# Kernel optimization log

Measured on AMD Instinct MI355X. Metric: run time of the kernel, lower is better.

Reference implementation:

```python
import jax, jax.numpy as jnp
import numpy as np

N, E, B = 50000, 800000, 64
ND, ED, HID, NC = 64, 16, 128, 6
HEADS = [4, 4, 1]
CH = [32, 32, 128]
CONCAT = [True, True, False]

PNAMES = ['pW', 'pb'] + [f'{p}{l}' for l in range(3) for p in ['W', 'as', 'ad', 'ae', 'We', 'b', 'g', 'be']] + ['gW1', 'gb1', 'gW2', 'gb2', 'cW1', 'cb1', 'cW2', 'cb2']


def _gat_conv(x, src, dst, ea, W, a_s, a_d, a_e, We, b, heads, ch, concat):
    n = x.shape[0]
    xp = (x @ W).reshape(n, heads, ch)          # [N,H,C]
    al_src = (xp * a_s).sum(-1)                 # [N,H]
    al_dst = (xp * a_d).sum(-1)                 # [N,H]
    ep = (ea @ We).reshape(-1, heads, ch)       # [E,H,C]
    al_edge = (ep * a_e).sum(-1)                # [E,H]
    alpha = jax.nn.leaky_relu(al_src[src] + al_dst[dst] + al_edge, 0.2)
    # segment softmax over destination nodes
    amax = jax.ops.segment_max(alpha, dst, num_segments=n)
    ex = jnp.exp(alpha - amax[dst])
    den = jax.ops.segment_sum(ex, dst, num_segments=n)
    alpha = ex / (den[dst] + 1e-16)
    out = jax.ops.segment_sum(xp[src] * alpha[:, :, None], dst, num_segments=n)
    out = out.reshape(n, heads * ch) if concat else out.mean(axis=1)
    return out + b


def _layernorm(x, g, be):
    m = x.mean(-1, keepdims=True)
    v = ((x - m) ** 2).mean(-1, keepdims=True)
    return (x - m) / jnp.sqrt(v + 1e-5) * g + be


def _forward(x, edge_index, edge_attr, batch, params):
    src, dst = edge_index[0], edge_index[1]
    h = jax.nn.relu(x @ params['pW'] + params['pb'])
    for l in range(3):
        r = h
        h = _gat_conv(h, src, dst, edge_attr, params[f'W{l}'], params[f'as{l}'],
                      params[f'ad{l}'], params[f'ae{l}'], params[f'We{l}'], params[f'b{l}'],
                      HEADS[l], CH[l], CONCAT[l])
        h = _layernorm(h, params[f'g{l}'], params[f'be{l}'])
        h = jax.nn.elu(h)
        h = h + r
    # GlobalAttention pooling: gate MLP + segment softmax over graphs
    gate = jax.nn.relu(h @ params['gW1'] + params['gb1']) @ params['gW2'] + params['gb2']  # [N,1]
    gmax = jax.ops.segment_max(gate, batch, num_segments=B)
    ge = jnp.exp(gate - gmax[batch])
    gden = jax.ops.segment_sum(ge, batch, num_segments=B)
    att = ge / (gden[batch] + 1e-16)
    pooled = jax.ops.segment_sum(att * h, batch, num_segments=B)  # [B,HID]
    return jax.nn.relu(pooled @ params['cW1'] + params['cb1']) @ params['cW2'] + params['cb2']


def setup_inputs() -> dict:
    key = jax.random.key(0)
    ks = iter(jax.random.split(key, 64))
    nx = lambda: next(ks)
    rn = lambda shape, s=0.1: jax.random.normal(nx(), shape, jnp.float32) * s
    inp = {
        'x': jax.random.normal(nx(), (N, ND), jnp.float32),
        'edge_index': jax.random.randint(nx(), (2, E), 0, N),
        'edge_attr': jax.random.normal(nx(), (E, ED), jnp.float32),
        'batch': jnp.sort(jax.random.randint(nx(), (N,), 0, B)),
        'pW': rn((ND, HID)), 'pb': jnp.zeros((HID,), jnp.float32),
    }
    for l in range(3):
        h, c = HEADS[l], CH[l]
        inp[f'W{l}'] = rn((HID, h * c))
        inp[f'as{l}'] = rn((h, c))
        inp[f'ad{l}'] = rn((h, c))
        inp[f'ae{l}'] = rn((h, c))
        inp[f'We{l}'] = rn((ED, h * c))
        inp[f'b{l}'] = jnp.zeros((HID,), jnp.float32)
        inp[f'g{l}'] = jnp.ones((HID,), jnp.float32)
        inp[f'be{l}'] = jnp.zeros((HID,), jnp.float32)
    inp['gW1'] = rn((HID, HID // 2)); inp['gb1'] = jnp.zeros((HID // 2,), jnp.float32)
    inp['gW2'] = rn((HID // 2, 1)); inp['gb2'] = jnp.zeros((1,), jnp.float32)
    inp['cW1'] = rn((HID, HID // 2)); inp['cb1'] = jnp.zeros((HID // 2,), jnp.float32)
    inp['cW2'] = rn((HID // 2, NC)); inp['cb2'] = jnp.zeros((NC,), jnp.float32)
    return inp


def reference(x, edge_index, edge_attr, batch, pW, pb,
              W0, as0, ad0, ae0, We0, b0, g0, be0,
              W1, as1, ad1, ae1, We1, b1, g1, be1,
              W2, as2, ad2, ae2, We2, b2, g2, be2,
              gW1, gb1, gW2, gb2, cW1, cb1, cW2, cb2):
    params = dict(zip(PNAMES, (pW, pb, W0, as0, ad0, ae0, We0, b0, g0, be0,
                               W1, as1, ad1, ae1, We1, b1, g1, be1,
                               W2, as2, ad2, ae2, We2, b2, g2, be2,
                               gW1, gb1, gW2, gb2, cW1, cb1, cW2, cb2)))
    return _forward(x, edge_index, edge_attr, batch, params)
```

## Files before the change

kernel.cpp:

```cpp
#include <hip/hip_runtime.h>
#include <hip/hip_fp16.h>
#include <math.h>

#define N_NODES 50000
#define N_EDGES 800000
#define NB      64
#define ND      64
#define ED      16
#define HID     128
#define NC      6
#define POOL_SPLIT 32
#define SCAN_BLOCKS ((N_NODES + 255) / 256)
#define GEMM_BLOCKS ((N_NODES + 63) / 64)

typedef _Float16 f16;
typedef f16  half8  __attribute__((ext_vector_type(8)));
typedef float floatx4 __attribute__((ext_vector_type(4)));

__global__ void k_setup(const float* __restrict__ pW, const float* __restrict__ W0,
                        const float* __restrict__ W1, const float* __restrict__ W2,
                        const float* __restrict__ We0, const float* __restrict__ ae0,
                        const float* __restrict__ We1, const float* __restrict__ ae1,
                        const float* __restrict__ We2, const float* __restrict__ ae2,
                        int* __restrict__ deg, float* __restrict__ pooled,
                        float* __restrict__ WeAe,
                        f16* __restrict__ Wtp, f16* __restrict__ Wt0,
                        f16* __restrict__ Wt1, f16* __restrict__ Wt2) {
    int i = blockIdx.x * 256 + threadIdx.x;
    if (i < N_NODES) deg[i] = 0;
    if (i < NB * HID) pooled[i] = 0.f;
    if (i < 128 * 64) {
        int n = i / 64, k = i % 64;
        Wtp[i] = (f16)pW[k * 128 + n];
    }
    if (i < 128 * 128) {
        int n = i / 128, k = i % 128;
        Wt0[i] = (f16)W0[k * 128 + n];
        Wt1[i] = (f16)W1[k * 128 + n];
        Wt2[i] = (f16)W2[k * 128 + n];
    }
    if (i >= 60000 && i < 60144) {
        int t = i - 60000;
        if (t < 64) {
            int k = t >> 2, h = t & 3;
            float s = 0.f;
            for (int c = 0; c < 32; c++) s += We0[k * HID + h * 32 + c] * ae0[h * 32 + c];
            WeAe[k * 9 + h] = s;
        } else if (t < 128) {
            int tt = t - 64;
            int k = tt >> 2, h = tt & 3;
            float s = 0.f;
            for (int c = 0; c < 32; c++) s += We1[k * HID + h * 32 + c] * ae1[h * 32 + c];
            WeAe[k * 9 + 4 + h] = s;
        } else {
            int k = t - 128;
            float s = 0.f;
            for (int c = 0; c < HID; c++) s += We2[k * HID + c] * ae2[c];
            WeAe[k * 9 + 8] = s;
        }
    }
}

template <int K, int MODE>
__global__ __launch_bounds__(256) void k_gemm(
        const float* __restrict__ act, const f16* __restrict__ Wt,
        const float* __restrict__ bias, const float* __restrict__ as_,
        const float* __restrict__ ad_, float* __restrict__ hout,
        __half* __restrict__ xp, float* __restrict__ al_src,
        float* __restrict__ al_dst) {
    constexpr int KP = K + 8;
    __shared__ __align__(16) f16 A[64 * KP];
    __shared__ float part_s[4][64];
    __shared__ float part_d[4][64];
    int tid = threadIdx.x;
    int base = blockIdx.x * 64;

    constexpr int NV = 64 * K / 4 / 256;
    #pragma unroll
    for (int i = 0; i < NV; i++) {
        int v = tid + i * 256;
        int row = v / (K / 4);
        int k4 = v % (K / 4);
        float4 xv = make_float4(0.f, 0.f, 0.f, 0.f);
        if (base + row < N_NODES)
            xv = *(const float4*)(act + (size_t)(base + row) * K + k4 * 4);
        f16* dp = &A[row * KP + k4 * 4];
        dp[0] = (f16)xv.x; dp[1] = (f16)xv.y; dp[2] = (f16)xv.z; dp[3] = (f16)xv.w;
    }
    __syncthreads();

    int w = tid >> 6, l = tid & 63;
    int lm = l & 15, q = l >> 4;
    floatx4 acc[4][2];
    #pragma unroll
    for (int mt = 0; mt < 4; mt++)
        #pragma unroll
        for (int j = 0; j < 2; j++)
            acc[mt][j] = (floatx4){0.f, 0.f, 0.f, 0.f};

    #pragma unroll
    for (int kt = 0; kt < K / 32; kt++) {
        int ko = kt * 32 + q * 8;
        half8 b0 = *(const half8*)(Wt + (size_t)(w * 32 + lm) * K + ko);
        half8 b1 = *(const half8*)(Wt + (size_t)(w * 32 + 16 + lm) * K + ko);
        #pragma unroll
        for (int mt = 0; mt < 4; mt++) {
            half8 a = *(const half8*)(&A[(mt * 16 + lm) * KP + ko]);
            acc[mt][0] = __builtin_amdgcn_mfma_f32_16x16x32_f16(a, b0, acc[mt][0], 0, 0, 0);
            acc[mt][1] = __builtin_amdgcn_mfma_f32_16x16x32_f16(a, b1, acc[mt][1], 0, 0, 0);
        }
    }

    if (MODE == 0) {
        float b0 = bias[w * 32 + lm];
        float b1 = bias[w * 32 + 16 + lm];
        #pragma unroll
        for (int mt = 0; mt < 4; mt++)
            #pragma unroll
            for (int r = 0; r < 4; r++) {
                int row = mt * 16 + q * 4 + r;
                if (base + row < N_NODES) {
                    hout[(size_t)(base + row) * HID + w * 32 + lm]      = fmaxf(acc[mt][0][r] + b0, 0.f);
                    hout[(size_t)(base + row) * HID + w * 32 + 16 + lm] = fmaxf(acc[mt][1][r] + b1, 0.f);
                }
            }
    } else {
        float a0 = as_[w * 32 + lm], a1 = as_[w * 32 + 16 + lm];
        float e0 = ad_[w * 32 + lm], e1 = ad_[w * 32 + 16 + lm];
        float ps[4][4], pd[4][4];
        #pragma unroll
        for (int mt = 0; mt < 4; mt++)
            #pragma unroll
            for (int r = 0; r < 4; r++) {
                ps[mt][r] = acc[mt][0][r] * a0 + acc[mt][1][r] * a1;
                pd[mt][r] = acc[mt][0][r] * e0 + acc[mt][1][r] * e1;
            }
        #pragma unroll
        for (int off = 1; off < 16; off <<= 1)
            #pragma unroll
            for (int mt = 0; mt < 4; mt++)
                #pragma unroll
                for (int r = 0; r < 4; r++) {
                    ps[mt][r] += __shfl_xor(ps[mt][r], off, 64);
                    pd[mt][r] += __shfl_xor(pd[mt][r], off, 64);
                }
        if (MODE == 1) {
            if (lm == 0)
                #pragma unroll
                for (int mt = 0; mt < 4; mt++)
                    #pragma unroll
                    for (int r = 0; r < 4; r++) {
                        int n = base + mt * 16 + q * 4 + r;
                        if (n < N_NODES) {
                            al_src[n * 4 + w] = ps[mt][r];
                            al_dst[n * 4 + w] = pd[mt][r];
                        }
                    }
        } else {
            if (lm == 0)
                #pragma unroll
                for (int mt = 0; mt < 4; mt++)
                    #pragma unroll
                    for (int r = 0; r < 4; r++) {
                        part_s[w][mt * 16 + q * 4 + r] = ps[mt][r];
                        part_d[w][mt * 16 + q * 4 + r] = pd[mt][r];
                    }
        }
        __syncthreads();
        #pragma unroll
        for (int mt = 0; mt < 4; mt++)
            #pragma unroll
            for (int r = 0; r < 4; r++) {
                int row = mt * 16 + q * 4 + r;
                A[row * KP + w * 32 + lm]      = (f16)acc[mt][0][r];
                A[row * KP + w * 32 + 16 + lm] = (f16)acc[mt][1][r];
            }
        if (MODE == 2 && tid < 64) {
            int n = base + tid;
            if (n < N_NODES) {
                al_src[n] = part_s[0][tid] + part_s[1][tid] + part_s[2][tid] + part_s[3][tid];
                al_dst[n] = part_d[0][tid] + part_d[1][tid] + part_d[2][tid] + part_d[3][tid];
            }
        }
        __syncthreads();
        #pragma unroll
        for (int i = 0; i < 4; i++) {
            int v = tid + i * 256;
            int row = v >> 4, c8 = v & 15;
            if (base + row < N_NODES) {
                float4 hv = *(const float4*)(&A[row * KP + c8 * 8]);
                *reinterpret_cast<float4*>(reinterpret_cast<char*>(xp) +
                    ((size_t)(base + row) * HID + c8 * 8) * 2) = hv;
            }
        }
    }
}

__global__ void k_deg(const int* __restrict__ dst, int* __restrict__ deg,
                      int* __restrict__ rank) {
    int e = blockIdx.x * blockDim.x + threadIdx.x;
    if (e < N_EDGES) rank[e] = atomicAdd(&deg[dst[e]], 1);
}

__global__ void k_scanA(const int* __restrict__ deg, int* __restrict__ bsum) {
    __shared__ int wsu[4];
    int t = threadIdx.x;
    int i = blockIdx.x * 256 + t;
    int d = (i < N_NODES) ? deg[i] : 0;
    int v = d;
    #pragma unroll
    for (int o = 32; o > 0; o >>= 1) v += __shfl_xor(v, o, 64);
    if ((t & 63) == 0) wsu[t >> 6] = v;
    __syncthreads();
    if (t == 0) bsum[blockIdx.x] = wsu[0] + wsu[1] + wsu[2] + wsu[3];
}

__global__ void k_scanB(const int* __restrict__ bsum, int* __restrict__ bpre,
                        int* __restrict__ offs) {
    __shared__ int sc[256];
    int t = threadIdx.x;
    int d = (t < SCAN_BLOCKS) ? bsum[t] : 0;
    sc[t] = d;
    __syncthreads();
    for (int o = 1; o < 256; o <<= 1) {
        int v = (t >= o) ? sc[t - o] : 0;
        __syncthreads();
        sc[t] += v;
        __syncthreads();
    }
    if (t < SCAN_BLOCKS) bpre[t] = sc[t] - d;
    if (t == 0) offs[N_NODES] = N_EDGES;
}

__global__ void k_scanC(const int* __restrict__ deg, const int* __restrict__ bpre,
                        int* __restrict__ offs) {
    __shared__ int sc[256];
    int t = threadIdx.x;
    int i = blockIdx.x * 256 + t;
    int d = (i < N_NODES) ? deg[i] : 0;
    sc[t] = d;
    __syncthreads();
    for (int o = 1; o < 256; o <<= 1) {
        int v = (t >= o) ? sc[t - o] : 0;
        __syncthreads();
        sc[t] += v;
        __syncthreads();
    }
    if (i < N_NODES) offs[i] = bpre[blockIdx.x] + sc[t] - d;
}

__global__ void k_edge_build(const int* __restrict__ src, const int* __restrict__ dst,
                             const int* __restrict__ rank, const int* __restrict__ offs,
                             const float* __restrict__ ea, const float* __restrict__ WeAe,
                             float4* __restrict__ rec) {
    __shared__ float w[ED * 9];
    __shared__ float4 rs[256][4];
    __shared__ int rp[256];
    int tid = threadIdx.x;
    if (tid < ED * 9) w[tid] = WeAe[tid];
    __syncthreads();
    int e = blockIdx.x * 256 + tid;
    if (e < N_EDGES) {
        float ev[ED];
        const float4* ep4 = reinterpret_cast<const float4*>(ea + (size_t)e * ED);
        #pragma unroll
        for (int q = 0; q < 4; q++) {
            float4 v = ep4[q];
            ev[q * 4 + 0] = v.x; ev[q * 4 + 1] = v.y;
            ev[q * 4 + 2] = v.z; ev[q * 4 + 3] = v.w;
        }
        float r[9];
        #pragma unroll
        for (int j = 0; j < 9; j++) r[j] = 0.f;
        #pragma unroll
        for (int k = 0; k < ED; k++) {
            float evk = ev[k];
            #pragma unroll
            for (int j = 0; j < 9; j++) r[j] += evk * w[k * 9 + j];
        }
        int d = dst[e], s = src[e];
        rp[tid] = offs[d] + rank[e];
        rs[tid][0] = make_float4(r[0], r[1], r[2], r[3]);
        rs[tid][1] = make_float4(r[4], r[5], r[6], r[7]);
        rs[tid][2] = make_float4(r[8], __int_as_float(s), __int_as_float(d), 0.f);
        rs[tid][3] = make_float4(0.f, 0.f, 0.f, 0.f);
    } else {
        rp[tid] = -1;
    }
    __syncthreads();
    int g0 = tid >> 2, q = tid & 3;
    #pragma unroll
    for (int rr = 0; rr < 4; rr++) {
        int g = rr * 64 + g0;
        int p = rp[g];
        if (p >= 0) rec[(size_t)p * 4 + q] = rs[g][q];
    }
}

template <int H, int SLOT>
__global__ void k_node_agg(const int* __restrict__ offs, const float4* __restrict__ rec,
                           const float* __restrict__ al_src, const float* __restrict__ al_dst,
                           const __half* __restrict__ xp, const float* __restrict__ bias,
                           const float* __restrict__ g, const float* __restrict__ be,
                           const float* __restrict__ hin, float* __restrict__ hout) {
    int tid = threadIdx.x;
    int wave = tid >> 6;
    int lane = tid & 63;
    int n = blockIdx.x * 4 + wave;
    if (n >= N_NODES) return;
    int e0 = offs[n], e1 = offs[n + 1];
    int side = lane >> 4;
    int cl = lane & 15;
    int c = cl * 8;
    int h = cl >> 2;
    float ald = (H == 4) ? al_dst[n * 4 + h] : al_dst[n];
    float acc[8] = {0.f, 0.f, 0.f, 0.f, 0.f, 0.f, 0.f, 0.f};
    float den = 0.f;

    auto fetchw = [&](int i, int& s, float& wv) {
        if (i < e1) {
            const float* rb = (const float*)(rec + (size_t)i * 4);
            s = __float_as_int(rb[9]);
            float r = (H == 4) ? rb[SLOT * 4 + h] : rb[8];
            float al = ((H == 4) ? al_src[s * 4 + h] : al_src[s]) + ald + r;
            al = (al >= 0.f) ? al : 0.2f * al;
            wv = __expf(al);
        } else { s = 0; wv = 0.f; }
    };
    auto accum = [&](uint4 r, float wv) {
        union { uint4 u; __half2 h2[4]; } t2; t2.u = r;
        #pragma unroll
        for (int j = 0; j < 4; j++) {
            float2 f = __half22float2(t2.h2[j]);
            acc[j * 2]     += wv * f.x;
            acc[j * 2 + 1] += wv * f.y;
        }
        den += wv;
    };

    int i = e0 + side;
    int sA, sB; float wA, wB;
    fetchw(i, sA, wA);
    fetchw(i + 4, sB, wB);
    while (i < e1) {
        uint4 rA = *reinterpret_cast<const uint4*>(xp + (size_t)sA * HID + c);
        uint4 rB = *reinterpret_cast<const uint4*>(xp + (size_t)sB * HID + c);
        int sC, sD; float wC, wD;
        fetchw(i + 8, sC, wC);
        fetchw(i + 12, sD, wD);
        accum(rA, wA);
        accum(rB, wB);
        sA = sC; wA = wC; sB = sD; wB = wD;
        i += 8;
    }
    #pragma unroll
    for (int j = 0; j < 8; j++) {
        acc[j] += __shfl_xor(acc[j], 16, 64);
        acc[j] += __shfl_xor(acc[j], 32, 64);
    }
    den += __shfl_xor(den, 16, 64);
    den += __shfl_xor(den, 32, 64);

    float inv = 1.f / (den + 1e-16f);
    float v[8];
    const float4 bv0 = *reinterpret_cast<const float4*>(bias + c);
    const float4 bv1 = *reinterpret_cast<const float4*>(bias + c + 4);
    v[0] = acc[0] * inv + bv0.x; v[1] = acc[1] * inv + bv0.y;
    v[2] = acc[2] * inv + bv0.z; v[3] = acc[3] * inv + bv0.w;
    v[4] = acc[4] * inv + bv1.x; v[5] = acc[5] * inv + bv1.y;
    v[6] = acc[6] * inv + bv1.z; v[7] = acc[7] * inv + bv1.w;
    float s8 = v[0] + v[1] + v[2] + v[3] + v[4] + v[5] + v[6] + v[7];
    #pragma unroll
    for (int o = 8; o > 0; o >>= 1) s8 += __shfl_xor(s8, o, 64);
    float mean = s8 * (1.f / HID);
    float q8 = 0.f;
    float d[8];
    #pragma unroll
    for (int j = 0; j < 8; j++) { d[j] = v[j] - mean; q8 += d[j] * d[j]; }
    #pragma unroll
    for (int o = 8; o > 0; o >>= 1) q8 += __shfl_xor(q8, o, 64);
    float rstd = rsqrtf(q8 * (1.f / HID) + 1e-5f);
    if (side < 2) {
        int co = c + side * 4;
        int j0 = side * 4;
        const float4 gv  = *reinterpret_cast<const float4*>(g + co);
        const float4 bev = *reinterpret_cast<const float4*>(be + co);
        float y0 = d[j0]     * rstd * gv.x + bev.x;
        float y1 = d[j0 + 1] * rstd * gv.y + bev.y;
        float y2 = d[j0 + 2] * rstd * gv.z + bev.z;
        float y3 = d[j0 + 3] * rstd * gv.w + bev.w;
        y0 = (y0 > 0.f) ? y0 : (__expf(y0) - 1.f);
        y1 = (y1 > 0.f) ? y1 : (__expf(y1) - 1.f);
        y2 = (y2 > 0.f) ? y2 : (__expf(y2) - 1.f);
        y3 = (y3 > 0.f) ? y3 : (__expf(y3) - 1.f);
        const float4 rv = *reinterpret_cast<const float4*>(hin + (size_t)n * HID + co);
        *reinterpret_cast<float4*>(hout + (size_t)n * HID + co) =
            make_float4(y0 + rv.x, y1 + rv.y, y2 + rv.z, y3 + rv.w);
    }
}

__global__ void k_gate(const float* __restrict__ h, const float* __restrict__ gW1,
                       const float* __restrict__ gb1, const float* __restrict__ gW2,
                       const float* __restrict__ gb2, const int* __restrict__ batch,
                       float* __restrict__ gate, int* __restrict__ goff) {
    __shared__ float hs[16][HID];
    int tid = threadIdx.x;
    int base = blockIdx.x * 16;
    if (tid < 16) {
        int n = base + tid;
        int cur = batch[n];
        int prev = (n == 0) ? -1 : batch[n - 1];
        for (int gg = prev + 1; gg <= cur; gg++) goff[gg] = n;
        if (n == N_NODES - 1)
            for (int gg = cur + 1; gg <= NB; gg++) goff[gg] = N_NODES;
    }
    for (int idx = tid; idx < 16 * HID; idx += 256) {
        int nn = idx >> 7, k = idx & 127;
        hs[nn][k] = h[(size_t)(base + nn) * HID + k];
    }
    __syncthreads();
    int c = tid & 63;
    int wave = tid >> 6;
    float acc[4] = {0.f, 0.f, 0.f, 0.f};
    #pragma unroll 8
    for (int k = 0; k < HID; k++) {
        float wv = gW1[k * 64 + c];
        #pragma unroll
        for (int q = 0; q < 4; q++) acc[q] += hs[wave * 4 + q][k] * wv;
    }
    float b1 = gb1[c], w2 = gW2[c];
    float p[4];
    #pragma unroll
    for (int q = 0; q < 4; q++) p[q] = fmaxf(acc[q] + b1, 0.f) * w2;
    #pragma unroll
    for (int o = 32; o > 0; o >>= 1) {
        #pragma unroll
        for (int q = 0; q < 4; q++) p[q] += __shfl_xor(p[q], o, 64);
    }
    if (c == 0) {
        float b2 = gb2[0];
        #pragma unroll
        for (int q = 0; q < 4; q++) gate[base + wave * 4 + q] = p[q] + b2;
    }
}

__global__ void k_gmaxden(const float* __restrict__ gate, const int* __restrict__ goff,
                          float* __restrict__ gmax, float* __restrict__ gden) {
    int b = blockIdx.x;
    int t = threadIdx.x;
    __shared__ float red[256];
    int s = goff[b], e = goff[b + 1];
    float m = -__builtin_inff();
    for (int n = s + t; n < e; n += 256) m = fmaxf(m, gate[n]);
    red[t] = m;
    __syncthreads();
    for (int o = 128; o > 0; o >>= 1) { if (t < o) red[t] = fmaxf(red[t], red[t + o]); __syncthreads(); }
    m = red[0];
    __syncthreads();
    float d = 0.f;
    for (int n = s + t; n < e; n += 256) d += __expf(gate[n] - m);
    red[t] = d;
    __syncthreads();
    for (int o = 128; o > 0; o >>= 1) { if (t < o) red[t] += red[t + o]; __syncthreads(); }
    if (t == 0) { gmax[b] = m; gden[b] = red[0]; }
}

__global__ void k_pool(const float* __restrict__ h, const float* __restrict__ gate,
                       const float* __restrict__ gmax, const float* __restrict__ gden,
                       const int* __restrict__ goff, float* __restrict__ pooled) {
    int b = blockIdx.x;
    int part = blockIdx.y;
    int c = threadIdx.x;
    int s = goff[b], e = goff[b + 1];
    float m = gmax[b];
    float dinv = 1.f / (gden[b] + 1e-16f);
    float acc = 0.f;
    for (int n = s + part; n < e; n += POOL_SPLIT) {
        float att = __expf(gate[n] - m) * dinv;
        acc += att * h[(size_t)n * HID + c];
    }
    atomicAdd(&pooled[b * HID + c], acc);
}

__global__ void k_head(const float* __restrict__ pooled, const float* __restrict__ cW1,
                       const float* __restrict__ cb1, const float* __restrict__ cW2,
                       const float* __restrict__ cb2, float* __restrict__ out) {
    int b = blockIdx.x;
    int t = threadIdx.x;
    __shared__ float pr[HID];
    __shared__ float tr[64];
    pr[t] = pooled[b * HID + t];
    pr[t + 64] = pooled[b * HID + t + 64];
    __syncthreads();
    float a = cb1[t];
    #pragma unroll 8
    for (int k = 0; k < HID; k++) a += pr[k] * cW1[k * 64 + t];
    tr[t] = fmaxf(a, 0.f);
    __syncthreads();
    if (t < NC) {
        float o = cb2[t];
        #pragma unroll
        for (int k = 0; k < 64; k++) o += tr[k] * cW2[k * NC + t];
        out[b * NC + t] = o;
    }
}

extern "C" void kernel_launch(void* const* d_in, const int* in_sizes, int n_in,
                              void* d_out, int out_size, void* d_ws, size_t ws_size,
                              hipStream_t stream) {
    (void)in_sizes; (void)n_in; (void)out_size; (void)ws_size;
    const float* x     = (const float*)d_in[0];
    const int*   ei    = (const int*)d_in[1];
    const float* ea    = (const float*)d_in[2];
    const int*   batch = (const int*)d_in[3];
    const float* pW    = (const float*)d_in[4];
    const float* pb    = (const float*)d_in[5];
    const float *W[3], *as_[3], *ad_[3], *ae_[3], *We[3], *bb[3], *gg[3], *be[3];
    for (int l = 0; l < 3; l++) {
        int base = 6 + 8 * l;
        W[l]   = (const float*)d_in[base + 0];
        as_[l] = (const float*)d_in[base + 1];
        ad_[l] = (const float*)d_in[base + 2];
        ae_[l] = (const float*)d_in[base + 3];
        We[l]  = (const float*)d_in[base + 4];
        bb[l]  = (const float*)d_in[base + 5];
        gg[l]  = (const float*)d_in[base + 6];
        be[l]  = (const float*)d_in[base + 7];
    }
    const float* gW1 = (const float*)d_in[30];
    const float* gb1 = (const float*)d_in[31];
    const float* gW2 = (const float*)d_in[32];
    const float* gb2 = (const float*)d_in[33];
    const float* cW1 = (const float*)d_in[34];
    const float* cb1 = (const float*)d_in[35];
    const float* cW2 = (const float*)d_in[36];
    const float* cb2 = (const float*)d_in[37];
    float* out = (float*)d_out;

    char* p = (char*)d_ws;
    auto take = [&](size_t bytes) -> char* {
        char* r = p;
        p += (bytes + 255) & ~(size_t)255;
        return r;
    };
    float*  h0      = (float*)take((size_t)N_NODES * HID * 4);
    float*  h1      = (float*)take((size_t)N_NODES * HID * 4);
    __half* xp      = (__half*)take((size_t)N_NODES * HID * 2);
    float*  al_src  = (float*)take((size_t)N_NODES * 4 * 4);
    float*  al_dst  = (float*)take((size_t)N_NODES * 4 * 4);
    float4* rec     = (float4*)take((size_t)N_EDGES * 64);
    int*    deg     = (int*)take((size_t)N_NODES * 4);
    int*    offs    = (int*)take((size_t)(N_NODES + 1) * 4);
    int*    rank    = (int*)take((size_t)N_EDGES * 4);
    int*    bsum    = (int*)take(256 * 4);
    int*    bpre    = (int*)take(256 * 4);
    float*  WeAe    = (float*)take(ED * 9 * 4);
    float*  gate    = (float*)take((size_t)N_NODES * 4);
    float*  gmax    = (float*)take(NB * 4);
    float*  gden    = (float*)take(NB * 4);
    int*    goff    = (int*)take((NB + 1) * 4);
    float*  pooled  = (float*)take(NB * HID * 4);
    f16*    Wtp     = (f16*)take(128 * 64 * 2);
    f16*    Wt0     = (f16*)take(128 * 128 * 2);
    f16*    Wt1     = (f16*)take(128 * 128 * 2);
    f16*    Wt2     = (f16*)take(128 * 128 * 2);
    f16*    Wt[3]   = {Wt0, Wt1, Wt2};

    const int* src = ei;
    const int* dst = ei + N_EDGES;

    k_setup<<<256, 256, 0, stream>>>(pW, W[0], W[1], W[2], We[0], ae_[0], We[1], ae_[1],
                                     We[2], ae_[2], deg, pooled, WeAe, Wtp, Wt0, Wt1, Wt2);
    k_gemm<64, 0><<<GEMM_BLOCKS, 256, 0, stream>>>(x, Wtp, pb, nullptr, nullptr,
                                                   h0, nullptr, nullptr, nullptr);
    k_deg<<<(N_EDGES + 255) / 256, 256, 0, stream>>>(dst, deg, rank);
    k_scanA<<<SCAN_BLOCKS, 256, 0, stream>>>(deg, bsum);
    k_scanB<<<1, 256, 0, stream>>>(bsum, bpre, offs);
    k_scanC<<<SCAN_BLOCKS, 256, 0, stream>>>(deg, bpre, offs);
    k_edge_build<<<(N_EDGES + 255) / 256, 256, 0, stream>>>(src, dst, rank, offs, ea, WeAe, rec);

    float* hc = h0;
    float* hn = h1;
    k_gemm<128, 1><<<GEMM_BLOCKS, 256, 0, stream>>>(hc, Wt[0], nullptr, as_[0], ad_[0],
                                                    nullptr, xp, al_src, al_dst);
    k_node_agg<4, 0><<<(N_NODES + 3) / 4, 256, 0, stream>>>(offs, rec, al_src, al_dst, xp,
                                                            bb[0], gg[0], be[0], hc, hn);
    { float* t = hc; hc = hn; hn = t; }
    k_gemm<128, 1><<<GEMM_BLOCKS, 256, 0, stream>>>(hc, Wt[1], nullptr, as_[1], ad_[1],
                                                    nullptr, xp, al_src, al_dst);
    k_node_agg<4, 1><<<(N_NODES + 3) / 4, 256, 0, stream>>>(offs, rec, al_src, al_dst, xp,
                                                            bb[1], gg[1], be[1], hc, hn);
    { float* t = hc; hc = hn; hn = t; }
    k_gemm<128, 2><<<GEMM_BLOCKS, 256, 0, stream>>>(hc, Wt[2], nullptr, as_[2], ad_[2],
                                                    nullptr, xp, al_src, al_dst);
    k_node_agg<1, 0><<<(N_NODES + 3) / 4, 256, 0, stream>>>(offs, rec, al_src, al_dst, xp,
                                                            bb[2], gg[2], be[2], hc, hn);
    { float* t = hc; hc = hn; hn = t; }

    k_gate<<<N_NODES / 16, 256, 0, stream>>>(hc, gW1, gb1, gW2, gb2, batch, gate, goff);
    k_gmaxden<<<NB, 256, 0, stream>>>(gate, goff, gmax, gden);
    k_pool<<<dim3(NB, POOL_SPLIT), HID, 0, stream>>>(hc, gate, gmax, gden, goff, pooled);
    k_head<<<NB, 64, 0, stream>>>(pooled, cW1, cb1, cW2, cb2, out);
}
```

Before: 494.9 us.

## Store hidden activations in fp16, fuse projection with degree count, merge scans, deepen gather prefetch

```diff
diff --git a/kernel.cpp b/kernel.cpp
--- a/kernel.cpp
+++ b/kernel.cpp
@@ -12,6 +12,7 @@
 #define POOL_SPLIT 32
 #define SCAN_BLOCKS ((N_NODES + 255) / 256)
 #define GEMM_BLOCKS ((N_NODES + 63) / 64)
+#define DEG_BLOCKS  ((N_EDGES + 255) / 256)
 
 typedef _Float16 f16;
 typedef f16  half8  __attribute__((ext_vector_type(8)));
@@ -61,31 +62,44 @@
     }
 }
 
-template <int K, int MODE>
-__global__ __launch_bounds__(256) void k_gemm(
-        const float* __restrict__ act, const f16* __restrict__ Wt,
+template <int K, int MODE, typename AT>
+__device__ __forceinline__ void gemm_body(
+        const AT* __restrict__ act, const f16* __restrict__ Wt,
         const float* __restrict__ bias, const float* __restrict__ as_,
-        const float* __restrict__ ad_, float* __restrict__ hout,
+        const float* __restrict__ ad_, __half* __restrict__ hout,
         __half* __restrict__ xp, float* __restrict__ al_src,
-        float* __restrict__ al_dst) {
+        float* __restrict__ al_dst, int blk) {
     constexpr int KP = K + 8;
-    __shared__ __align__(16) f16 A[64 * KP];
+    constexpr int OP = HID + 8;
+    __shared__ __align__(16) f16 A[64 * OP];
     __shared__ float part_s[4][64];
     __shared__ float part_d[4][64];
     int tid = threadIdx.x;
-    int base = blockIdx.x * 64;
-
-    constexpr int NV = 64 * K / 4 / 256;
-    #pragma unroll
-    for (int i = 0; i < NV; i++) {
-        int v = tid + i * 256;
-        int row = v / (K / 4);
-        int k4 = v % (K / 4);
-        float4 xv = make_float4(0.f, 0.f, 0.f, 0.f);
-        if (base + row < N_NODES)
-            xv = *(const float4*)(act + (size_t)(base + row) * K + k4 * 4);
-        f16* dp = &A[row * KP + k4 * 4];
-        dp[0] = (f16)xv.x; dp[1] = (f16)xv.y; dp[2] = (f16)xv.z; dp[3] = (f16)xv.w;
+    int base = blk * 64;
+
+    if constexpr (sizeof(AT) == 4) {
+        constexpr int NV = 64 * (K / 4) / 256;
+        #pragma unroll
+        for (int i = 0; i < NV; i++) {
+            int v = tid + i * 256;
+            int row = v / (K / 4), k4 = v % (K / 4);
+            float4 xv = make_float4(0.f, 0.f, 0.f, 0.f);
+            if (base + row < N_NODES)
+                xv = *(const float4*)((const float*)act + (size_t)(base + row) * K + k4 * 4);
+            f16* dp = &A[row * KP + k4 * 4];
+            dp[0] = (f16)xv.x; dp[1] = (f16)xv.y; dp[2] = (f16)xv.z; dp[3] = (f16)xv.w;
+        }
+    } else {
+        constexpr int NV = 64 * (K / 8) / 256;
+        #pragma unroll
+        for (int i = 0; i < NV; i++) {
+            int v = tid + i * 256;
+            int row = v / (K / 8), k8 = v % (K / 8);
+            uint4 xv = make_uint4(0, 0, 0, 0);
+            if (base + row < N_NODES)
+                xv = *(const uint4*)((const __half*)act + (size_t)(base + row) * K + k8 * 8);
+            *(uint4*)(&A[row * KP + k8 * 8]) = xv;
+        }
     }
     __syncthreads();
 
@@ -114,16 +128,26 @@
     if (MODE == 0) {
         float b0 = bias[w * 32 + lm];
         float b1 = bias[w * 32 + 16 + lm];
+        __syncthreads();
         #pragma unroll
         for (int mt = 0; mt < 4; mt++)
             #pragma unroll
             for (int r = 0; r < 4; r++) {
                 int row = mt * 16 + q * 4 + r;
-                if (base + row < N_NODES) {
-                    hout[(size_t)(base + row) * HID + w * 32 + lm]      = fmaxf(acc[mt][0][r] + b0, 0.f);
-                    hout[(size_t)(base + row) * HID + w * 32 + 16 + lm] = fmaxf(acc[mt][1][r] + b1, 0.f);
-                }
+                A[row * OP + w * 32 + lm]      = (f16)fmaxf(acc[mt][0][r] + b0, 0.f);
+                A[row * OP + w * 32 + 16 + lm] = (f16)fmaxf(acc[mt][1][r] + b1, 0.f);
             }
+        __syncthreads();
+        #pragma unroll
+        for (int i = 0; i < 4; i++) {
+            int v = tid + i * 256;
+            int row = v >> 4, c8 = v & 15;
+            if (base + row < N_NODES) {
+                float4 hv = *(const float4*)(&A[row * OP + c8 * 8]);
+                *reinterpret_cast<float4*>(reinterpret_cast<char*>(hout) +
+                    ((size_t)(base + row) * HID + c8 * 8) * 2) = hv;
+            }
+        }
     } else {
         float a0 = as_[w * 32 + lm], a1 = as_[w * 32 + 16 + lm];
         float e0 = ad_[w * 32 + lm], e1 = ad_[w * 32 + 16 + lm];
@@ -172,8 +196,8 @@
             #pragma unroll
             for (int r = 0; r < 4; r++) {
                 int row = mt * 16 + q * 4 + r;
-                A[row * KP + w * 32 + lm]      = (f16)acc[mt][0][r];
-                A[row * KP + w * 32 + 16 + lm] = (f16)acc[mt][1][r];
+                A[row * OP + w * 32 + lm]      = (f16)acc[mt][0][r];
+                A[row * OP + w * 32 + 16 + lm] = (f16)acc[mt][1][r];
             }
         if (MODE == 2 && tid < 64) {
             int n = base + tid;
@@ -188,7 +212,7 @@
             int v = tid + i * 256;
             int row = v >> 4, c8 = v & 15;
             if (base + row < N_NODES) {
-                float4 hv = *(const float4*)(&A[row * KP + c8 * 8]);
+                float4 hv = *(const float4*)(&A[row * OP + c8 * 8]);
                 *reinterpret_cast<float4*>(reinterpret_cast<char*>(xp) +
                     ((size_t)(base + row) * HID + c8 * 8) * 2) = hv;
             }
@@ -196,10 +220,26 @@
     }
 }
 
-__global__ void k_deg(const int* __restrict__ dst, int* __restrict__ deg,
-                      int* __restrict__ rank) {
-    int e = blockIdx.x * blockDim.x + threadIdx.x;
-    if (e < N_EDGES) rank[e] = atomicAdd(&deg[dst[e]], 1);
+__global__ __launch_bounds__(256) void k_proj_deg(
+        const float* __restrict__ x, const f16* __restrict__ Wtp,
+        const float* __restrict__ pb, __half* __restrict__ h,
+        const int* __restrict__ dst, int* __restrict__ deg, int* __restrict__ rank) {
+    if (blockIdx.x < GEMM_BLOCKS) {
+        gemm_body<64, 0, float>(x, Wtp, pb, nullptr, nullptr, h, nullptr, nullptr, nullptr,
+                                blockIdx.x);
+    } else {
+        int e = (blockIdx.x - GEMM_BLOCKS) * 256 + threadIdx.x;
+        if (e < N_EDGES) rank[e] = atomicAdd(&deg[dst[e]], 1);
+    }
+}
+
+template <int K, int MODE>
+__global__ __launch_bounds__(256) void k_gemm(
+        const __half* __restrict__ act, const f16* __restrict__ Wt,
+        const float* __restrict__ as_, const float* __restrict__ ad_,
+        __half* __restrict__ xp, float* __restrict__ al_src, float* __restrict__ al_dst) {
+    gemm_body<K, MODE, __half>(act, Wt, nullptr, as_, ad_, nullptr, xp, al_src, al_dst,
+                               blockIdx.x);
 }
 
 __global__ void k_scanA(const int* __restrict__ deg, int* __restrict__ bsum) {
@@ -215,11 +255,19 @@
     if (t == 0) bsum[blockIdx.x] = wsu[0] + wsu[1] + wsu[2] + wsu[3];
 }
 
-__global__ void k_scanB(const int* __restrict__ bsum, int* __restrict__ bpre,
-                        int* __restrict__ offs) {
+__global__ void k_scanC2(const int* __restrict__ deg, const int* __restrict__ bsum,
+                         int* __restrict__ offs) {
     __shared__ int sc[256];
+    __shared__ int wred[4];
     int t = threadIdx.x;
-    int d = (t < SCAN_BLOCKS) ? bsum[t] : 0;
+    int b = (t < (int)blockIdx.x) ? bsum[t] : 0;
+    #pragma unroll
+    for (int o = 32; o > 0; o >>= 1) b += __shfl_xor(b, o, 64);
+    if ((t & 63) == 0) wred[t >> 6] = b;
+    __syncthreads();
+    int pre = wred[0] + wred[1] + wred[2] + wred[3];
+    int i = blockIdx.x * 256 + t;
+    int d = (i < N_NODES) ? deg[i] : 0;
     sc[t] = d;
     __syncthreads();
     for (int o = 1; o < 256; o <<= 1) {
@@ -228,25 +276,8 @@
         sc[t] += v;
         __syncthreads();
     }
-    if (t < SCAN_BLOCKS) bpre[t] = sc[t] - d;
-    if (t == 0) offs[N_NODES] = N_EDGES;
-}
-
-__global__ void k_scanC(const int* __restrict__ deg, const int* __restrict__ bpre,
-                        int* __restrict__ offs) {
-    __shared__ int sc[256];
-    int t = threadIdx.x;
-    int i = blockIdx.x * 256 + t;
-    int d = (i < N_NODES) ? deg[i] : 0;
-    sc[t] = d;
-    __syncthreads();
-    for (int o = 1; o < 256; o <<= 1) {
-        int v = (t >= o) ? sc[t - o] : 0;
-        __syncthreads();
-        sc[t] += v;
-        __syncthreads();
-    }
-    if (i < N_NODES) offs[i] = bpre[blockIdx.x] + sc[t] - d;
+    if (i < N_NODES) offs[i] = pre + sc[t] - d;
+    if (i == 0) offs[N_NODES] = N_EDGES;
 }
 
 __global__ void k_edge_build(const int* __restrict__ src, const int* __restrict__ dst,
@@ -302,7 +333,7 @@
                            const float* __restrict__ al_src, const float* __restrict__ al_dst,
                            const __half* __restrict__ xp, const float* __restrict__ bias,
                            const float* __restrict__ g, const float* __restrict__ be,
-                           const float* __restrict__ hin, float* __restrict__ hout) {
+                           const __half* __restrict__ hin, __half* __restrict__ hout) {
     int tid = threadIdx.x;
     int wave = tid >> 6;
     int lane = tid & 63;
@@ -339,19 +370,28 @@
     };
 
     int i = e0 + side;
-    int sA, sB; float wA, wB;
+    int sA, sB, sC, sD; float wA, wB, wC, wD;
     fetchw(i, sA, wA);
     fetchw(i + 4, sB, wB);
+    fetchw(i + 8, sC, wC);
+    fetchw(i + 12, sD, wD);
     while (i < e1) {
         uint4 rA = *reinterpret_cast<const uint4*>(xp + (size_t)sA * HID + c);
         uint4 rB = *reinterpret_cast<const uint4*>(xp + (size_t)sB * HID + c);
-        int sC, sD; float wC, wD;
-        fetchw(i + 8, sC, wC);
-        fetchw(i + 12, sD, wD);
+        uint4 rC = *reinterpret_cast<const uint4*>(xp + (size_t)sC * HID + c);
+        uint4 rD = *reinterpret_cast<const uint4*>(xp + (size_t)sD * HID + c);
+        int tA, tB, tC, tD; float vA, vB, vC, vD;
+        fetchw(i + 16, tA, vA);
+        fetchw(i + 20, tB, vB);
+        fetchw(i + 24, tC, vC);
+        fetchw(i + 28, tD, vD);
         accum(rA, wA);
         accum(rB, wB);
-        sA = sC; wA = wC; sB = sD; wB = wD;
-        i += 8;
+        accum(rC, wC);
+        accum(rD, wD);
+        sA = tA; wA = vA; sB = tB; wB = vB;
+        sC = tC; wC = vC; sD = tD; wD = vD;
+        i += 16;
     }
     #pragma unroll
     for (int j = 0; j < 8; j++) {
@@ -393,13 +433,18 @@
         y1 = (y1 > 0.f) ? y1 : (__expf(y1) - 1.f);
         y2 = (y2 > 0.f) ? y2 : (__expf(y2) - 1.f);
         y3 = (y3 > 0.f) ? y3 : (__expf(y3) - 1.f);
-        const float4 rv = *reinterpret_cast<const float4*>(hin + (size_t)n * HID + co);
-        *reinterpret_cast<float4*>(hout + (size_t)n * HID + co) =
-            make_float4(y0 + rv.x, y1 + rv.y, y2 + rv.z, y3 + rv.w);
-    }
-}
-
-__global__ void k_gate(const float* __restrict__ h, const float* __restrict__ gW1,
+        uint2 ru = *reinterpret_cast<const uint2*>(hin + (size_t)n * HID + co);
+        union { uint2 u; __half2 h2[2]; } tr; tr.u = ru;
+        float2 r01 = __half22float2(tr.h2[0]);
+        float2 r23 = __half22float2(tr.h2[1]);
+        union { uint2 u; __half2 h2[2]; } to;
+        to.h2[0] = __floats2half2_rn(y0 + r01.x, y1 + r01.y);
+        to.h2[1] = __floats2half2_rn(y2 + r23.x, y3 + r23.y);
+        *reinterpret_cast<uint2*>(hout + (size_t)n * HID + co) = to.u;
+    }
+}
+
+__global__ void k_gate(const __half* __restrict__ h, const float* __restrict__ gW1,
                        const float* __restrict__ gb1, const float* __restrict__ gW2,
                        const float* __restrict__ gb2, const int* __restrict__ batch,
                        float* __restrict__ gate, int* __restrict__ goff) {
@@ -414,9 +459,16 @@
         if (n == N_NODES - 1)
             for (int gg = cur + 1; gg <= NB; gg++) goff[gg] = N_NODES;
     }
-    for (int idx = tid; idx < 16 * HID; idx += 256) {
-        int nn = idx >> 7, k = idx & 127;
-        hs[nn][k] = h[(size_t)(base + nn) * HID + k];
+    {
+        int nn = tid >> 4, k8 = tid & 15;
+        uint4 hv = *reinterpret_cast<const uint4*>(h + (size_t)(base + nn) * HID + k8 * 8);
+        union { uint4 u; __half2 h2[4]; } th; th.u = hv;
+        #pragma unroll
+        for (int j = 0; j < 4; j++) {
+            float2 f = __half22float2(th.h2[j]);
+            hs[nn][k8 * 8 + j * 2]     = f.x;
+            hs[nn][k8 * 8 + j * 2 + 1] = f.y;
+        }
     }
     __syncthreads();
     int c = tid & 63;
@@ -465,7 +517,7 @@
     if (t == 0) { gmax[b] = m; gden[b] = red[0]; }
 }
 
-__global__ void k_pool(const float* __restrict__ h, const float* __restrict__ gate,
+__global__ void k_pool(const __half* __restrict__ h, const float* __restrict__ gate,
                        const float* __restrict__ gmax, const float* __restrict__ gden,
                        const int* __restrict__ goff, float* __restrict__ pooled) {
     int b = blockIdx.x;
@@ -477,7 +529,7 @@
     float acc = 0.f;
     for (int n = s + part; n < e; n += POOL_SPLIT) {
         float att = __expf(gate[n] - m) * dinv;
-        acc += att * h[(size_t)n * HID + c];
+        acc += att * __half2float(h[(size_t)n * HID + c]);
     }
     atomicAdd(&pooled[b * HID + c], acc);
 }
@@ -543,8 +595,8 @@
         p += (bytes + 255) & ~(size_t)255;
         return r;
     };
-    float*  h0      = (float*)take((size_t)N_NODES * HID * 4);
-    float*  h1      = (float*)take((size_t)N_NODES * HID * 4);
+    __half* h0      = (__half*)take((size_t)N_NODES * HID * 2);
+    __half* h1      = (__half*)take((size_t)N_NODES * HID * 2);
     __half* xp      = (__half*)take((size_t)N_NODES * HID * 2);
     float*  al_src  = (float*)take((size_t)N_NODES * 4 * 4);
     float*  al_dst  = (float*)take((size_t)N_NODES * 4 * 4);
@@ -553,7 +605,6 @@
     int*    offs    = (int*)take((size_t)(N_NODES + 1) * 4);
     int*    rank    = (int*)take((size_t)N_EDGES * 4);
     int*    bsum    = (int*)take(256 * 4);
-    int*    bpre    = (int*)take(256 * 4);
     float*  WeAe    = (float*)take(ED * 9 * 4);
     float*  gate    = (float*)take((size_t)N_NODES * 4);
     float*  gmax    = (float*)take(NB * 4);
@@ -571,31 +622,25 @@
 
     k_setup<<<256, 256, 0, stream>>>(pW, W[0], W[1], W[2], We[0], ae_[0], We[1], ae_[1],
                                      We[2], ae_[2], deg, pooled, WeAe, Wtp, Wt0, Wt1, Wt2);
-    k_gemm<64, 0><<<GEMM_BLOCKS, 256, 0, stream>>>(x, Wtp, pb, nullptr, nullptr,
-                                                   h0, nullptr, nullptr, nullptr);
-    k_deg<<<(N_EDGES + 255) / 256, 256, 0, stream>>>(dst, deg, rank);
+    k_proj_deg<<<GEMM_BLOCKS + DEG_BLOCKS, 256, 0, stream>>>(x, Wtp, pb, h0, dst, deg, rank);
     k_scanA<<<SCAN_BLOCKS, 256, 0, stream>>>(deg, bsum);
-    k_scanB<<<1, 256, 0, stream>>>(bsum, bpre, offs);
-    k_scanC<<<SCAN_BLOCKS, 256, 0, stream>>>(deg, bpre, offs);
-    k_edge_build<<<(N_EDGES + 255) / 256, 256, 0, stream>>>(src, dst, rank, offs, ea, WeAe, rec);
-
-    float* hc = h0;
-    float* hn = h1;
-    k_gemm<128, 1><<<GEMM_BLOCKS, 256, 0, stream>>>(hc, Wt[0], nullptr, as_[0], ad_[0],
-                                                    nullptr, xp, al_src, al_dst);
+    k_scanC2<<<SCAN_BLOCKS, 256, 0, stream>>>(deg, bsum, offs);
+    k_edge_build<<<DEG_BLOCKS, 256, 0, stream>>>(src, dst, rank, offs, ea, WeAe, rec);
+
+    __half* hc = h0;
+    __half* hn = h1;
+    k_gemm<128, 1><<<GEMM_BLOCKS, 256, 0, stream>>>(hc, Wt[0], as_[0], ad_[0], xp, al_src, al_dst);
     k_node_agg<4, 0><<<(N_NODES + 3) / 4, 256, 0, stream>>>(offs, rec, al_src, al_dst, xp,
                                                             bb[0], gg[0], be[0], hc, hn);
-    { float* t = hc; hc = hn; hn = t; }
-    k_gemm<128, 1><<<GEMM_BLOCKS, 256, 0, stream>>>(hc, Wt[1], nullptr, as_[1], ad_[1],
-                                                    nullptr, xp, al_src, al_dst);
+    { __half* t = hc; hc = hn; hn = t; }
+    k_gemm<128, 1><<<GEMM_BLOCKS, 256, 0, stream>>>(hc, Wt[1], as_[1], ad_[1], xp, al_src, al_dst);
     k_node_agg<4, 1><<<(N_NODES + 3) / 4, 256, 0, stream>>>(offs, rec, al_src, al_dst, xp,
                                                             bb[1], gg[1], be[1], hc, hn);
-    { float* t = hc; hc = hn; hn = t; }
-    k_gemm<128, 2><<<GEMM_BLOCKS, 256, 0, stream>>>(hc, Wt[2], nullptr, as_[2], ad_[2],
-                                                    nullptr, xp, al_src, al_dst);
+    { __half* t = hc; hc = hn; hn = t; }
+    k_gemm<128, 2><<<GEMM_BLOCKS, 256, 0, stream>>>(hc, Wt[2], as_[2], ad_[2], xp, al_src, al_dst);
     k_node_agg<1, 0><<<(N_NODES + 3) / 4, 256, 0, stream>>>(offs, rec, al_src, al_dst, xp,
                                                             bb[2], gg[2], be[2], hc, hn);
-    { float* t = hc; hc = hn; hn = t; }
+    { __half* t = hc; hc = hn; hn = t; }
 
     k_gate<<<N_NODES / 16, 256, 0, stream>>>(hc, gW1, gb1, gW2, gb2, batch, gate, goff);
     k_gmaxden<<<NB, 256, 0, stream>>>(gate, goff, gmax, gden);
```

Result: faster. 484.0 us (-2.2%).
